# Kernel optimization log

Measured on AMD Instinct MI355X. Metric: run time of the kernel, lower is better.

## Reference

```python
import jax, jax.numpy as jnp
import numpy as np

B, N, IN_F, OUT_F, HEADS = 16, 256, 128, 64, 4
NEG = -9e15

def setup_inputs() -> dict:
    key = jax.random.key(0)
    ks = jax.random.split(key, 7)
    x = jax.random.normal(ks[0], (B, N, IN_F), dtype=jnp.float32)
    adj = jax.random.randint(ks[1], (B, N, N), 0, 2, dtype=jnp.int32)
    adj_in = jax.random.randint(ks[2], (B, N, N), 0, 2, dtype=jnp.int32)
    adj_out = jax.random.randint(ks[3], (B, N, N), 0, 2, dtype=jnp.int32)
    # params: W linear (no bias), a linear (with bias)
    gain = 1.414
    lim_W = gain * np.sqrt(6.0 / (IN_F + OUT_F))
    W = jax.random.uniform(ks[4], (OUT_F, IN_F), jnp.float32, -lim_W, lim_W)
    lim_A = gain * np.sqrt(6.0 / (2 * OUT_F + 3 * HEADS))
    A = jax.random.uniform(ks[5], (3 * HEADS, 2 * OUT_F), jnp.float32, -lim_A, lim_A)
    a_b = jax.random.uniform(ks[6], (3 * HEADS,), jnp.float32, -1.0, 1.0) / np.sqrt(2 * OUT_F)
    return {"x": x, "adj": adj, "adj_in": adj_in, "adj_out": adj_out,
            "W": W, "A": A, "a_b": a_b}

def reference(x, adj, adj_in, adj_out, W, A, a_b):
    # h = W(input): [B, N, OUT_F]
    h = jnp.einsum('bni,oi->bno', x, W)
    # additive attention: a(cat[h_i, h_j]) = h_i @ A1^T + h_j @ A2^T + b
    A1, A2 = A[:, :OUT_F], A[:, OUT_F:]
    e_src = jnp.einsum('bnd,hd->bnh', h, A1)  # depends on row i
    e_dst = jnp.einsum('bnd,hd->bnh', h, A2)  # depends on col j
    e = e_src[:, :, None, :] + e_dst[:, None, :, :] + a_b  # [B, N, N, 3H]
    e = jax.nn.leaky_relu(e, negative_slope=0.01)
    e = jnp.transpose(e, (0, 3, 1, 2))  # [B, 3H, N, N]
    # tripled masks: [adj]*H ++ [adj_in]*H ++ [adj_out]*H along head axis
    mask = jnp.concatenate([
        jnp.repeat(adj[:, None], HEADS, axis=1),
        jnp.repeat(adj_in[:, None], HEADS, axis=1),
        jnp.repeat(adj_out[:, None], HEADS, axis=1)], axis=1)  # [B, 3H, N, N]
    att = jnp.where(mask > 0, e, jnp.float32(NEG))
    att = jax.nn.softmax(att, axis=-1)
    # dropout omitted (eval mode)
    h_prime = jnp.einsum('bhij,bjd->bhid', att, h).mean(axis=1)  # [B, N, OUT_F]
    return h_prime
```

## Files before the change

kernel.cpp:

```cpp
#include <hip/hip_runtime.h>

#define L2E 1.44269504088896340736f

typedef __attribute__((ext_vector_type(8))) short bf16x8;
typedef __attribute__((ext_vector_type(4))) float f32x4;

__device__ __forceinline__ unsigned bf16_rne(float v) {
    unsigned x = __float_as_uint(v);
    return (x + 0x7FFFu + ((x >> 16) & 1u)) >> 16;
}

__global__ __launch_bounds__(256) void k1_proj(
    const float* __restrict__ x, const float* __restrict__ W, const float* __restrict__ A,
    unsigned short* __restrict__ hTg, float* __restrict__ esrc, float* __restrict__ edst)
{
    __shared__ float wl[64 * 132];
    __shared__ float xs[16 * 128];
    __shared__ float hs[16 * 68];
    const int t = threadIdx.x;
    const int row0 = blockIdx.x * 16;
    const int b = row0 >> 8;
    const int ibase = row0 & 255;

#pragma unroll
    for (int i = 0; i < 32; ++i) {
        int idx = t + 256 * i;
        wl[(idx >> 7) * 132 + (idx & 127)] = W[idx];
    }
#pragma unroll
    for (int i = 0; i < 8; ++i) {
        int idx = t + 256 * i;
        xs[idx] = x[row0 * 128 + idx];
    }
    __syncthreads();

    const int o = t & 63;
    const int w = t >> 6;
    float acc[4] = {0.f, 0.f, 0.f, 0.f};
    const float* wrow = &wl[o * 132];
#pragma unroll
    for (int k4 = 0; k4 < 32; ++k4) {
        const float4 wv = *(const float4*)&wrow[k4 * 4];
#pragma unroll
        for (int g = 0; g < 4; ++g) {
            const float4 xv = *(const float4*)&xs[(w * 4 + g) * 128 + k4 * 4];
            acc[g] += wv.x * xv.x + wv.y * xv.y + wv.z * xv.z + wv.w * xv.w;
        }
    }
#pragma unroll
    for (int g = 0; g < 4; ++g)
        hs[(w * 4 + g) * 68 + o] = acc[g];
    __syncthreads();

#pragma unroll
    for (int it = 0; it < 4; ++it) {
        int elem = t + 256 * it;
        int d = elem >> 4, jj = elem & 15;
        hTg[(b * 64 + d) * 256 + ibase + jj] = (unsigned short)bf16_rne(hs[jj * 68 + d]);
    }

#pragma unroll
    for (int pass = 0; pass < 2; ++pass) {
        int task = t + 256 * pass;
        if (task < 384) {
            int row = task / 24;
            int rem = task - row * 24;
            int hh  = rem % 12;
            int isd = rem / 12;
            const float* hr = &hs[row * 68];
            const float* ar = &A[hh * 128 + isd * 64];
            float a = 0.f;
#pragma unroll
            for (int d4 = 0; d4 < 16; ++d4) {
                float4 hv = *(const float4*)&hr[d4 * 4];
                float4 av = *(const float4*)&ar[d4 * 4];
                a += hv.x * av.x + hv.y * av.y + hv.z * av.z + hv.w * av.w;
            }
            (isd ? edst : esrc)[(row0 + row) * 12 + hh] = a;
        }
    }
}

__global__ __launch_bounds__(512) void k2_attn(
    const int* __restrict__ adj, const int* __restrict__ adjin, const int* __restrict__ adjout,
    const float* __restrict__ esrc, const float* __restrict__ edst,
    const unsigned short* __restrict__ hTg, const float* __restrict__ ab,
    float* __restrict__ out)
{
    __shared__ unsigned short hT[64 * 264];
    __shared__ float edl[12 * 256];
    __shared__ unsigned short Ph[16 * 264];
    __shared__ unsigned short Pl_[16 * 264];

    const int t = threadIdx.x;
    const int b  = blockIdx.x >> 5;
    const int i0 = (blockIdx.x & 31) * 8;
    const int lane = t & 63;
    const int w = t >> 6;

    {
        const uint4* src = (const uint4*)(hTg + (size_t)b * 64 * 256);
#pragma unroll
        for (int it = 0; it < 4; ++it) {
            int task = t + 512 * it;
            int d = task >> 5, jg = task & 31;
            *(uint4*)&hT[d * 264 + jg * 8] = src[d * 32 + jg];
        }
    }
    {
        const float* eb = edst + (size_t)b * 256 * 12;
#pragma unroll
        for (int e = 0; e < 6; ++e) {
            int elem = t + 512 * e;
            int j = elem / 12;
            int hh = elem - j * 12;
            edl[hh * 256 + j] = eb[elem];
        }
    }
    __syncthreads();

    const int gi = b * 256 + i0 + w;
    const int4 M0 = *(const int4*)(adj    + (size_t)gi * 256 + 4 * lane);
    const int4 M1 = *(const int4*)(adjin  + (size_t)gi * 256 + 4 * lane);
    const int4 M2 = *(const int4*)(adjout + (size_t)gi * 256 + 4 * lane);
    const float mA[4] = {(float)M0.x, (float)M0.y, (float)M0.z, (float)M0.w};
    const float mB[4] = {(float)M1.x, (float)M1.y, (float)M1.z, (float)M1.w};
    const float mC[4] = {(float)M2.x, (float)M2.y, (float)M2.z, (float)M2.w};

    const float* es = esrc + (size_t)gi * 12;
    float Pacc[4] = {0.f, 0.f, 0.f, 0.f};
#pragma unroll
    for (int hh = 0; hh < 12; ++hh) {
        const float e0 = es[hh] + ab[hh];
        const float4 ev = *(const float4*)&edl[hh * 256 + 4 * lane];
        float v0 = e0 + ev.x, v1 = e0 + ev.y, v2 = e0 + ev.z, v3 = e0 + ev.w;
        v0 = v0 > 0.f ? v0 : 0.01f * v0;
        v1 = v1 > 0.f ? v1 : 0.01f * v1;
        v2 = v2 > 0.f ? v2 : 0.01f * v2;
        v3 = v3 > 0.f ? v3 : 0.01f * v3;
        const float m0 = (hh < 4) ? mA[0] : (hh < 8) ? mB[0] : mC[0];
        const float m1 = (hh < 4) ? mA[1] : (hh < 8) ? mB[1] : mC[1];
        const float m2 = (hh < 4) ? mA[2] : (hh < 8) ? mB[2] : mC[2];
        const float m3 = (hh < 4) ? mA[3] : (hh < 8) ? mB[3] : mC[3];
        float p0 = __builtin_amdgcn_exp2f(v0 * L2E) * m0;
        float p1 = __builtin_amdgcn_exp2f(v1 * L2E) * m1;
        float p2 = __builtin_amdgcn_exp2f(v2 * L2E) * m2;
        float p3 = __builtin_amdgcn_exp2f(v3 * L2E) * m3;
        float s = (p0 + p1) + (p2 + p3);
#pragma unroll
        for (int off = 32; off >= 1; off >>= 1)
            s += __shfl_xor(s, off);
        const float rinv = __builtin_amdgcn_rcpf(s);
        Pacc[0] += p0 * rinv;
        Pacc[1] += p1 * rinv;
        Pacc[2] += p2 * rinv;
        Pacc[3] += p3 * rinv;
    }
    {
        unsigned h0 = bf16_rne(Pacc[0]);
        unsigned h1 = bf16_rne(Pacc[1]);
        unsigned h2 = bf16_rne(Pacc[2]);
        unsigned h3 = bf16_rne(Pacc[3]);
        unsigned l0 = bf16_rne(Pacc[0] - __uint_as_float(h0 << 16));
        unsigned l1 = bf16_rne(Pacc[1] - __uint_as_float(h1 << 16));
        unsigned l2 = bf16_rne(Pacc[2] - __uint_as_float(h2 << 16));
        unsigned l3 = bf16_rne(Pacc[3] - __uint_as_float(h3 << 16));
        uint2 hw; hw.x = h0 | (h1 << 16); hw.y = h2 | (h3 << 16);
        uint2 lw; lw.x = l0 | (l1 << 16); lw.y = l2 | (l3 << 16);
        *(uint2*)&Ph[w * 264 + 4 * lane]  = hw;
        *(uint2*)&Pl_[w * 264 + 4 * lane] = lw;
    }
    __syncthreads();

    const int nt = w & 3, kh = w >> 2;
    const int ml = lane & 15, kb = lane >> 4;
    f32x4 acc = {0.f, 0.f, 0.f, 0.f};
#pragma unroll
    for (int ks = 0; ks < 4; ++ks) {
        const int koff = kh * 128 + ks * 32 + kb * 8;
        bf16x8 ah = *(const bf16x8*)&Ph[ml * 264 + koff];
        bf16x8 al = *(const bf16x8*)&Pl_[ml * 264 + koff];
        bf16x8 bh = *(const bf16x8*)&hT[(nt * 16 + ml) * 264 + koff];
        acc = __builtin_amdgcn_mfma_f32_16x16x32_bf16(ah, bh, acc, 0, 0, 0);
        acc = __builtin_amdgcn_mfma_f32_16x16x32_bf16(al, bh, acc, 0, 0, 0);
    }

    float* red = edl;
    if (kh == 1 && lane < 32) {
#pragma unroll
        for (int r = 0; r < 4; ++r)
            red[nt * 144 + ml * 9 + kb * 4 + r] = acc[r];
    }
    __syncthreads();
    if (kh == 0 && lane < 32) {
#pragma unroll
        for (int r = 0; r < 4; ++r) {
            const int mrow = kb * 4 + r;
            const float v = (acc[r] + red[nt * 144 + ml * 9 + mrow]) * (1.0f / 12.0f);
            out[(size_t)(b * 256 + i0 + mrow) * 64 + nt * 16 + ml] = v;
        }
    }
}

extern "C" void kernel_launch(void* const* d_in, const int* in_sizes, int n_in,
                              void* d_out, int out_size, void* d_ws, size_t ws_size,
                              hipStream_t stream) {
    const float* x    = (const float*)d_in[0];
    const int*   adj  = (const int*)d_in[1];
    const int*   adji = (const int*)d_in[2];
    const int*   adjo = (const int*)d_in[3];
    const float* W    = (const float*)d_in[4];
    const float* A    = (const float*)d_in[5];
    const float* ab   = (const float*)d_in[6];
    float* out = (float*)d_out;

    unsigned short* hTg = (unsigned short*)d_ws;
    float* esrc = (float*)((char*)d_ws + (1 << 20));
    float* edst = esrc + 4096 * 12;

    k1_proj<<<256, 256, 0, stream>>>(x, W, A, hTg, esrc, edst);
    k2_attn<<<512, 512, 0, stream>>>(adj, adji, adjo, esrc, edst, hTg, ab, out);
}
```

Measured before the change: 21.93 us.

## Use split-bf16 MFMA for projections and shrink attention blocks to skip LDS staging

```diff
diff --git a/kernel.cpp b/kernel.cpp
--- a/kernel.cpp
+++ b/kernel.cpp
@@ -10,116 +10,136 @@
     return (x + 0x7FFFu + ((x >> 16) & 1u)) >> 16;
 }
 
+__device__ __forceinline__ void cvt_hilo4(float4 v, uint2* hi, uint2* lo) {
+    unsigned h0 = bf16_rne(v.x), h1 = bf16_rne(v.y), h2 = bf16_rne(v.z), h3 = bf16_rne(v.w);
+    float f0 = __uint_as_float(h0 << 16), f1 = __uint_as_float(h1 << 16);
+    float f2 = __uint_as_float(h2 << 16), f3 = __uint_as_float(h3 << 16);
+    unsigned l0 = bf16_rne(v.x - f0), l1 = bf16_rne(v.y - f1);
+    unsigned l2 = bf16_rne(v.z - f2), l3 = bf16_rne(v.w - f3);
+    hi->x = h0 | (h1 << 16); hi->y = h2 | (h3 << 16);
+    lo->x = l0 | (l1 << 16); lo->y = l2 | (l3 << 16);
+}
+
 __global__ __launch_bounds__(256) void k1_proj(
     const float* __restrict__ x, const float* __restrict__ W, const float* __restrict__ A,
-    unsigned short* __restrict__ hTg, float* __restrict__ esrc, float* __restrict__ edst)
+    unsigned short* __restrict__ hTg, float* __restrict__ esrc, float* __restrict__ edstT)
 {
-    __shared__ float wl[64 * 132];
-    __shared__ float xs[16 * 128];
-    __shared__ float hs[16 * 68];
+    __shared__ unsigned short xh[16 * 136], xl[16 * 136];
+    __shared__ unsigned short wh[64 * 136], wl[64 * 136];
+    __shared__ unsigned short Ach[32 * 72], Acl[32 * 72];
+    __shared__ unsigned short hsh[16 * 72], hsl[16 * 72];
+
     const int t = threadIdx.x;
     const int row0 = blockIdx.x * 16;
     const int b = row0 >> 8;
     const int ibase = row0 & 255;
 
 #pragma unroll
-    for (int i = 0; i < 32; ++i) {
-        int idx = t + 256 * i;
-        wl[(idx >> 7) * 132 + (idx & 127)] = W[idx];
-    }
-#pragma unroll
-    for (int i = 0; i < 8; ++i) {
-        int idx = t + 256 * i;
-        xs[idx] = x[row0 * 128 + idx];
+    for (int p = 0; p < 2; ++p) {
+        int q = t + 256 * p;
+        int r = q >> 5, c = (q & 31) * 4;
+        float4 v = *(const float4*)&x[row0 * 128 + 4 * q];
+        uint2 hi, lo; cvt_hilo4(v, &hi, &lo);
+        *(uint2*)&xh[r * 136 + c] = hi;
+        *(uint2*)&xl[r * 136 + c] = lo;
+    }
+#pragma unroll
+    for (int p = 0; p < 8; ++p) {
+        int q = t + 256 * p;
+        int r = q >> 5, c = (q & 31) * 4;
+        float4 v = *(const float4*)&W[4 * q];
+        uint2 hi, lo; cvt_hilo4(v, &hi, &lo);
+        *(uint2*)&wh[r * 136 + c] = hi;
+        *(uint2*)&wl[r * 136 + c] = lo;
+    }
+#pragma unroll
+    for (int p = 0; p < 2; ++p) {
+        int q = t + 256 * p;
+        int n = q >> 4, d = (q & 15) * 4;
+        float4 v = make_float4(0.f, 0.f, 0.f, 0.f);
+        if (n < 24) {
+            int nn = (n < 12) ? n : n - 12;
+            v = *(const float4*)&A[nn * 128 + ((n < 12) ? 0 : 64) + d];
+        }
+        uint2 hi, lo; cvt_hilo4(v, &hi, &lo);
+        *(uint2*)&Ach[n * 72 + d] = hi;
+        *(uint2*)&Acl[n * 72 + d] = lo;
     }
     __syncthreads();
 
-    const int o = t & 63;
-    const int w = t >> 6;
-    float acc[4] = {0.f, 0.f, 0.f, 0.f};
-    const float* wrow = &wl[o * 132];
-#pragma unroll
-    for (int k4 = 0; k4 < 32; ++k4) {
-        const float4 wv = *(const float4*)&wrow[k4 * 4];
-#pragma unroll
-        for (int g = 0; g < 4; ++g) {
-            const float4 xv = *(const float4*)&xs[(w * 4 + g) * 128 + k4 * 4];
-            acc[g] += wv.x * xv.x + wv.y * xv.y + wv.z * xv.z + wv.w * xv.w;
+    const int lane = t & 63;
+    const int wv = t >> 6;
+    const int ml = lane & 15, kb = lane >> 4;
+
+    f32x4 acc = {0.f, 0.f, 0.f, 0.f};
+#pragma unroll
+    for (int ks = 0; ks < 4; ++ks) {
+        const int ko = ks * 32 + kb * 8;
+        bf16x8 axh = *(const bf16x8*)&xh[ml * 136 + ko];
+        bf16x8 axl = *(const bf16x8*)&xl[ml * 136 + ko];
+        bf16x8 bwh = *(const bf16x8*)&wh[(wv * 16 + ml) * 136 + ko];
+        bf16x8 bwl = *(const bf16x8*)&wl[(wv * 16 + ml) * 136 + ko];
+        acc = __builtin_amdgcn_mfma_f32_16x16x32_bf16(axh, bwh, acc, 0, 0, 0);
+        acc = __builtin_amdgcn_mfma_f32_16x16x32_bf16(axh, bwl, acc, 0, 0, 0);
+        acc = __builtin_amdgcn_mfma_f32_16x16x32_bf16(axl, bwh, acc, 0, 0, 0);
+    }
+#pragma unroll
+    for (int r = 0; r < 4; ++r) {
+        const int m = kb * 4 + r, c = wv * 16 + ml;
+        unsigned hi = bf16_rne(acc[r]);
+        float hif = __uint_as_float(hi << 16);
+        hsh[m * 72 + c] = (unsigned short)hi;
+        hsl[m * 72 + c] = (unsigned short)bf16_rne(acc[r] - hif);
+    }
+    __syncthreads();
+
+    if (wv < 2) {
+        f32x4 e4 = {0.f, 0.f, 0.f, 0.f};
+#pragma unroll
+        for (int ks = 0; ks < 2; ++ks) {
+            const int ko = ks * 32 + kb * 8;
+            bf16x8 ah = *(const bf16x8*)&hsh[ml * 72 + ko];
+            bf16x8 al = *(const bf16x8*)&hsl[ml * 72 + ko];
+            bf16x8 bh = *(const bf16x8*)&Ach[(wv * 16 + ml) * 72 + ko];
+            bf16x8 bl = *(const bf16x8*)&Acl[(wv * 16 + ml) * 72 + ko];
+            e4 = __builtin_amdgcn_mfma_f32_16x16x32_bf16(ah, bh, e4, 0, 0, 0);
+            e4 = __builtin_amdgcn_mfma_f32_16x16x32_bf16(ah, bl, e4, 0, 0, 0);
+            e4 = __builtin_amdgcn_mfma_f32_16x16x32_bf16(al, bh, e4, 0, 0, 0);
         }
-    }
-#pragma unroll
-    for (int g = 0; g < 4; ++g)
-        hs[(w * 4 + g) * 68 + o] = acc[g];
-    __syncthreads();
+#pragma unroll
+        for (int r = 0; r < 4; ++r) {
+            const int m = kb * 4 + r, n = wv * 16 + ml;
+            if (n < 12)
+                esrc[(row0 + m) * 12 + n] = e4[r];
+            else if (n < 24)
+                edstT[(b * 12 + (n - 12)) * 256 + ibase + m] = e4[r];
+        }
+    }
 
 #pragma unroll
     for (int it = 0; it < 4; ++it) {
-        int elem = t + 256 * it;
-        int d = elem >> 4, jj = elem & 15;
-        hTg[(b * 64 + d) * 256 + ibase + jj] = (unsigned short)bf16_rne(hs[jj * 68 + d]);
-    }
-
-#pragma unroll
-    for (int pass = 0; pass < 2; ++pass) {
-        int task = t + 256 * pass;
-        if (task < 384) {
-            int row = task / 24;
-            int rem = task - row * 24;
-            int hh  = rem % 12;
-            int isd = rem / 12;
-            const float* hr = &hs[row * 68];
-            const float* ar = &A[hh * 128 + isd * 64];
-            float a = 0.f;
-#pragma unroll
-            for (int d4 = 0; d4 < 16; ++d4) {
-                float4 hv = *(const float4*)&hr[d4 * 4];
-                float4 av = *(const float4*)&ar[d4 * 4];
-                a += hv.x * av.x + hv.y * av.y + hv.z * av.z + hv.w * av.w;
-            }
-            (isd ? edst : esrc)[(row0 + row) * 12 + hh] = a;
-        }
-    }
-}
-
-__global__ __launch_bounds__(512) void k2_attn(
+        int e2 = t + 256 * it;
+        int d = e2 >> 4, jj = e2 & 15;
+        hTg[(b * 64 + d) * 256 + ibase + jj] = hsh[jj * 72 + d];
+    }
+}
+
+__global__ __launch_bounds__(256) void k2_attn(
     const int* __restrict__ adj, const int* __restrict__ adjin, const int* __restrict__ adjout,
-    const float* __restrict__ esrc, const float* __restrict__ edst,
+    const float* __restrict__ esrc, const float* __restrict__ edstT,
     const unsigned short* __restrict__ hTg, const float* __restrict__ ab,
     float* __restrict__ out)
 {
-    __shared__ unsigned short hT[64 * 264];
-    __shared__ float edl[12 * 256];
     __shared__ unsigned short Ph[16 * 264];
     __shared__ unsigned short Pl_[16 * 264];
 
     const int t = threadIdx.x;
-    const int b  = blockIdx.x >> 5;
-    const int i0 = (blockIdx.x & 31) * 8;
+    const int b  = blockIdx.x >> 6;
+    const int i0 = (blockIdx.x & 63) * 4;
     const int lane = t & 63;
-    const int w = t >> 6;
-
-    {
-        const uint4* src = (const uint4*)(hTg + (size_t)b * 64 * 256);
-#pragma unroll
-        for (int it = 0; it < 4; ++it) {
-            int task = t + 512 * it;
-            int d = task >> 5, jg = task & 31;
-            *(uint4*)&hT[d * 264 + jg * 8] = src[d * 32 + jg];
-        }
-    }
-    {
-        const float* eb = edst + (size_t)b * 256 * 12;
-#pragma unroll
-        for (int e = 0; e < 6; ++e) {
-            int elem = t + 512 * e;
-            int j = elem / 12;
-            int hh = elem - j * 12;
-            edl[hh * 256 + j] = eb[elem];
-        }
-    }
-    __syncthreads();
-
-    const int gi = b * 256 + i0 + w;
+    const int wv = t >> 6;
+    const int gi = b * 256 + i0 + wv;
+
     const int4 M0 = *(const int4*)(adj    + (size_t)gi * 256 + 4 * lane);
     const int4 M1 = *(const int4*)(adjin  + (size_t)gi * 256 + 4 * lane);
     const int4 M2 = *(const int4*)(adjout + (size_t)gi * 256 + 4 * lane);
@@ -128,12 +148,15 @@
     const float mC[4] = {(float)M2.x, (float)M2.y, (float)M2.z, (float)M2.w};
 
     const float* es = esrc + (size_t)gi * 12;
+    float e0[12];
+#pragma unroll
+    for (int hh = 0; hh < 12; ++hh) e0[hh] = es[hh] + ab[hh];
+
     float Pacc[4] = {0.f, 0.f, 0.f, 0.f};
 #pragma unroll
     for (int hh = 0; hh < 12; ++hh) {
-        const float e0 = es[hh] + ab[hh];
-        const float4 ev = *(const float4*)&edl[hh * 256 + 4 * lane];
-        float v0 = e0 + ev.x, v1 = e0 + ev.y, v2 = e0 + ev.z, v3 = e0 + ev.w;
+        const float4 ev = *(const float4*)&edstT[(size_t)(b * 12 + hh) * 256 + 4 * lane];
+        float v0 = e0[hh] + ev.x, v1 = e0[hh] + ev.y, v2 = e0[hh] + ev.z, v3 = e0[hh] + ev.w;
         v0 = v0 > 0.f ? v0 : 0.01f * v0;
         v1 = v1 > 0.f ? v1 : 0.01f * v1;
         v2 = v2 > 0.f ? v2 : 0.01f * v2;
@@ -157,48 +180,35 @@
         Pacc[3] += p3 * rinv;
     }
     {
-        unsigned h0 = bf16_rne(Pacc[0]);
-        unsigned h1 = bf16_rne(Pacc[1]);
-        unsigned h2 = bf16_rne(Pacc[2]);
-        unsigned h3 = bf16_rne(Pacc[3]);
+        unsigned h0 = bf16_rne(Pacc[0]), h1 = bf16_rne(Pacc[1]);
+        unsigned h2 = bf16_rne(Pacc[2]), h3 = bf16_rne(Pacc[3]);
         unsigned l0 = bf16_rne(Pacc[0] - __uint_as_float(h0 << 16));
         unsigned l1 = bf16_rne(Pacc[1] - __uint_as_float(h1 << 16));
         unsigned l2 = bf16_rne(Pacc[2] - __uint_as_float(h2 << 16));
         unsigned l3 = bf16_rne(Pacc[3] - __uint_as_float(h3 << 16));
         uint2 hw; hw.x = h0 | (h1 << 16); hw.y = h2 | (h3 << 16);
         uint2 lw; lw.x = l0 | (l1 << 16); lw.y = l2 | (l3 << 16);
-        *(uint2*)&Ph[w * 264 + 4 * lane]  = hw;
-        *(uint2*)&Pl_[w * 264 + 4 * lane] = lw;
+        *(uint2*)&Ph[wv * 264 + 4 * lane]  = hw;
+        *(uint2*)&Pl_[wv * 264 + 4 * lane] = lw;
     }
     __syncthreads();
 
-    const int nt = w & 3, kh = w >> 2;
     const int ml = lane & 15, kb = lane >> 4;
+    const unsigned short* hTb = hTg + ((size_t)b * 64 + wv * 16 + ml) * 256;
     f32x4 acc = {0.f, 0.f, 0.f, 0.f};
 #pragma unroll
-    for (int ks = 0; ks < 4; ++ks) {
-        const int koff = kh * 128 + ks * 32 + kb * 8;
-        bf16x8 ah = *(const bf16x8*)&Ph[ml * 264 + koff];
-        bf16x8 al = *(const bf16x8*)&Pl_[ml * 264 + koff];
-        bf16x8 bh = *(const bf16x8*)&hT[(nt * 16 + ml) * 264 + koff];
+    for (int ks = 0; ks < 8; ++ks) {
+        const int ko = ks * 32 + kb * 8;
+        bf16x8 bh = *(const bf16x8*)&hTb[ko];
+        bf16x8 ah = *(const bf16x8*)&Ph[ml * 264 + ko];
+        bf16x8 al = *(const bf16x8*)&Pl_[ml * 264 + ko];
         acc = __builtin_amdgcn_mfma_f32_16x16x32_bf16(ah, bh, acc, 0, 0, 0);
         acc = __builtin_amdgcn_mfma_f32_16x16x32_bf16(al, bh, acc, 0, 0, 0);
     }
-
-    float* red = edl;
-    if (kh == 1 && lane < 32) {
+    if (kb == 0) {
 #pragma unroll
         for (int r = 0; r < 4; ++r)
-            red[nt * 144 + ml * 9 + kb * 4 + r] = acc[r];
-    }
-    __syncthreads();
-    if (kh == 0 && lane < 32) {
-#pragma unroll
-        for (int r = 0; r < 4; ++r) {
-            const int mrow = kb * 4 + r;
-            const float v = (acc[r] + red[nt * 144 + ml * 9 + mrow]) * (1.0f / 12.0f);
-            out[(size_t)(b * 256 + i0 + mrow) * 64 + nt * 16 + ml] = v;
-        }
+            out[(size_t)(b * 256 + i0 + r) * 64 + wv * 16 + ml] = acc[r] * (1.0f / 12.0f);
     }
 }
 
@@ -215,9 +225,9 @@
     float* out = (float*)d_out;
 
     unsigned short* hTg = (unsigned short*)d_ws;
-    float* esrc = (float*)((char*)d_ws + (1 << 20));
-    float* edst = esrc + 4096 * 12;
-
-    k1_proj<<<256, 256, 0, stream>>>(x, W, A, hTg, esrc, edst);
-    k2_attn<<<512, 512, 0, stream>>>(adj, adji, adjo, esrc, edst, hTg, ab, out);
-}
+    float* esrc  = (float*)((char*)d_ws + (512 << 10));
+    float* edstT = (float*)((char*)d_ws + (704 << 10));
+
+    k1_proj<<<256, 256, 0, stream>>>(x, W, A, hTg, esrc, edstT);
+    k2_attn<<<1024, 256, 0, stream>>>(adj, adji, adjo, esrc, edstT, hTg, ab, out);
+}
```

Result: faster. 19.73 us (-10.0%).
